# Performance work log

Measured on AMD Instinct MI355X. Metric: run time of the kernel, lower is better.

The kernel has to match this reference:

```python
import jax, jax.numpy as jnp
import numpy as np
import math

NUM_HEADS = 32
NUM_KV_HEADS = 8
HEAD_DIM = 128
SCALE = 1.0 / math.sqrt(128.0)
MAX_SEQLEN = 1152  # static max sequence length for padding
CU = [0, 1024, 1920, 3072, 4096]  # cumulative seq lens, batch=4
NUM_SLOTS = 8192  # 32 blocks * block_size 256


def setup_inputs() -> dict:
    key = jax.random.key(0)
    k0, k1, k2 = jax.random.split(key, 3)
    T = CU[-1]
    q = jax.random.normal(k0, (T, NUM_HEADS, HEAD_DIM), jnp.float32)
    k = jax.random.normal(k1, (T, NUM_KV_HEADS, HEAD_DIM), jnp.float32)
    v = jax.random.normal(k2, (T, NUM_KV_HEADS, HEAD_DIM), jnp.float32)
    k_cache = jnp.zeros((NUM_SLOTS, NUM_KV_HEADS, HEAD_DIM), jnp.float32)
    v_cache = jnp.zeros((NUM_SLOTS, NUM_KV_HEADS, HEAD_DIM), jnp.float32)
    cu_seqlens = jnp.array(CU, dtype=jnp.int32)
    slot_mapping = jnp.arange(T, dtype=jnp.int32)
    return {"q": q, "k": k, "v": v, "k_cache": k_cache, "v_cache": v_cache,
            "cu_seqlens": cu_seqlens, "slot_mapping": slot_mapping}


def _store_kv(key, value, k_cache, v_cache, slot_mapping):
    # scatter new K/V into paged cache; slot == -1 means skip
    valid = slot_mapping >= 0
    safe = jnp.where(valid, slot_mapping, 0)
    k_cache = k_cache.at[safe].set(
        jnp.where(valid[:, None, None], key, k_cache[safe]), mode='drop')
    v_cache = v_cache.at[safe].set(
        jnp.where(valid[:, None, None], value, v_cache[safe]), mode='drop')
    return k_cache, v_cache


def _prefill_attention(q, k, v, cu_seqlens):
    T = q.shape[0]
    B = cu_seqlens.shape[0] - 1
    groups = NUM_HEADS // NUM_KV_HEADS
    k = jnp.repeat(k, groups, axis=1)  # GQA expand -> [T, H, D]
    v = jnp.repeat(v, groups, axis=1)

    lens = cu_seqlens[1:] - cu_seqlens[:-1]            # [B]
    s = jnp.arange(MAX_SEQLEN)
    idx = cu_seqlens[:-1][:, None] + s[None, :]        # [B, S] packed token index
    valid = s[None, :] < lens[:, None]                 # [B, S]
    idx_safe = jnp.where(valid, idx, 0)

    # pack -> padded [B, S, H, D], zeroing pad positions
    qp = jnp.where(valid[..., None, None], q[idx_safe], 0.0)
    kp = jnp.where(valid[..., None, None], k[idx_safe], 0.0)
    vp = jnp.where(valid[..., None, None], v[idx_safe], 0.0)

    scores = jnp.einsum('bqhd,bkhd->bhqk', qp, kp) * SCALE  # [B, H, S, S]
    causal = s[:, None] >= s[None, :]                       # [S, S]
    mask = (causal[None, :, :] & valid[:, :, None] & valid[:, None, :])[:, None, :, :]
    scores = jnp.where(mask, scores, jnp.finfo(scores.dtype).min)
    attn = jax.nn.softmax(scores, axis=-1)
    outp = jnp.einsum('bhqk,bkhd->bqhd', attn, vp)          # [B, S, H, D]

    # unpack padded -> packed [T, H, D]
    tok = jnp.arange(T)
    seq_id = jnp.searchsorted(cu_seqlens, tok, side='right') - 1
    pos = tok - cu_seqlens[seq_id]
    return outp[seq_id, pos]


def reference(q, k, v, k_cache, v_cache, cu_seqlens, slot_mapping):
    k_cache, v_cache = _store_kv(k, v, k_cache, v_cache, slot_mapping)
    out = _prefill_attention(q, k, v, cu_seqlens)
    return out, k_cache, v_cache
```

## Files before the change

kernel.cpp:

```cpp
#include <hip/hip_runtime.h>
#include <hip/hip_bf16.h>

#define T_TOT   4096
#define NH      32
#define NKV     8
#define GQ      4
#define DHEAD   128
#define NSLOTS  8192
#define QB      64
#define QW      32
#define KVB     64
#define NTILES  (T_TOT / KVB)
#define ATT_SCALE 0.088388347648318447f

typedef __attribute__((ext_vector_type(8))) short bf16x8;
typedef __attribute__((ext_vector_type(4))) float f32x4;

__device__ __forceinline__ unsigned short f2bf(float f) {
    union { float f; unsigned u; } x; x.f = f;
    unsigned r = x.u + 0x7fffu + ((x.u >> 16) & 1u);
    return (unsigned short)(r >> 16);
}

__device__ __forceinline__ unsigned long long pack4bf(float a, float b, float c, float d) {
    unsigned lo = (unsigned)f2bf(a) | ((unsigned)f2bf(b) << 16);
    unsigned hi = (unsigned)f2bf(c) | ((unsigned)f2bf(d) << 16);
    return (unsigned long long)lo | ((unsigned long long)hi << 32);
}

__device__ __forceinline__ void gload16(const char* g, char* l) {
    __builtin_amdgcn_global_load_lds(
        (const __attribute__((address_space(1))) void*)g,
        (__attribute__((address_space(3))) void*)l,
        16, 0, 0);
}

__constant__ unsigned char QORD[64] = {
    47,46,15,45,63,14,44,62,13,29,43,61,12,28,42,60,
    11,27,41,59,10,26,40,58, 9,25,39,57, 8,24,38,56,
     7,23,37,55, 6,22,36,54, 5,21,35,53, 4,20,34,52,
     3,19,33,51, 2,18,32,50, 1,17,31,49, 0,16,30,48
};


__global__ __launch_bounds__(256) void copy_cache(const float4* __restrict__ kc,
                                                  const float4* __restrict__ vc,
                                                  float4* __restrict__ kco,
                                                  float4* __restrict__ vco) {
    int idx = blockIdx.x * 256 + threadIdx.x;
    kco[idx] = kc[idx];
    vco[idx] = vc[idx];
}

__global__ __launch_bounds__(256) void scatter_kv(const float4* __restrict__ k,
                                                  const float4* __restrict__ v,
                                                  const int* __restrict__ slot_map,
                                                  float4* __restrict__ kco,
                                                  float4* __restrict__ vco) {
    int idx = blockIdx.x * 256 + threadIdx.x;
    int tok = idx >> 8;
    int j   = idx & 255;
    int slot = slot_map[tok];
    if (slot >= 0 && slot < NSLOTS) {
        size_t dst = (size_t)slot * 256 + j;
        kco[dst] = k[idx];
        vco[dst] = v[idx];
    }
}


__global__ __launch_bounds__(256) void prep_kv(const float* __restrict__ kg,
                                               const float* __restrict__ vg,
                                               char* __restrict__ kbf,
                                               char* __restrict__ vbf) {
    const int tile = blockIdx.x;
    const int kvh  = blockIdx.y;
    const int tid  = threadIdx.x;
    char* kt = kbf + (((size_t)kvh * NTILES + tile) << 14);
    char* vt = vbf + (((size_t)kvh * NTILES + tile) << 14);
    #pragma unroll
    for (int it = 0; it < 8; ++it) {
        int idx = tid + it * 256;
        int key = idx >> 5, d4 = idx & 31;
        float4 x = *(const float4*)(kg +
            ((size_t)(tile * 64 + key) * NKV + kvh) * DHEAD + d4 * 4);
        *(unsigned long long*)(kt + key * 256 + ((d4 * 8) ^ ((key & 7) << 4))) =
            pack4bf(x.x, x.y, x.z, x.w);
    }
    #pragma unroll
    for (int it = 0; it < 8; ++it) {
        int job = tid + it * 256;
        int kq = job >> 7, d = job & 127;
        const float* vp = vg +
            ((size_t)(tile * 64 + kq * 4) * NKV + kvh) * DHEAD + d;
        *(unsigned long long*)(vt + d * 128 + ((kq * 8) ^ ((d & 15) << 3))) =
            pack4bf(vp[0], vp[NKV * DHEAD], vp[2 * NKV * DHEAD], vp[3 * NKV * DHEAD]);
    }
}


__global__ __launch_bounds__(512, 2) void attn_kernel(const float* __restrict__ qg,
                                                      const char* __restrict__ kbf,
                                                      const char* __restrict__ vbf,
                                                      const int* __restrict__ cu,
                                                      float* __restrict__ outg)
{
    __shared__ __align__(16) char Klds[KVB * 256];
    __shared__ __align__(16) char Vt[DHEAD * 128];
    __shared__ __align__(16) char Plds[8][QW * 128];

    const int tid  = threadIdx.x;
    const int wave = tid >> 6;
    const int lane = tid & 63;
    const int q16  = lane & 15;
    const int grp  = lane >> 4;
    const int bid  = blockIdx.x;
    const int qblk = QORD[bid >> 3];
    const int kvh  = bid & 7;
    const int head = kvh * GQ + (wave >> 1);
    const int tok0 = qblk * QB;
    const int qw0  = tok0 + (wave & 1) * QW;

    int seq_start = 0;
    #pragma unroll
    for (int b = 0; b < 4; ++b) {
        int c0 = cu[b], c1 = cu[b + 1];
        if (tok0 >= c0 && tok0 < c1) seq_start = c0;
    }
    const int p0  = tok0 - seq_start;
    const int pw0 = p0 + (wave & 1) * QW;
    const int ntiles = p0 / KVB + 1;
    const int tile0 = seq_start >> 6;

    bf16x8 qf[2][4];
    {
        const float* qp = qg + ((size_t)(qw0 + q16) * NH + head) * DHEAD + grp * 8;
        #pragma unroll
        for (int qt = 0; qt < 2; ++qt) {
            #pragma unroll
            for (int c = 0; c < 4; ++c) {
                const float* p = qp + (size_t)qt * 16 * NH * DHEAD + c * 32;
                float4 a = *(const float4*)(p);
                float4 b = *(const float4*)(p + 4);
                union { bf16x8 v; unsigned long long q[2]; } u;
                u.q[0] = pack4bf(a.x, a.y, a.z, a.w);
                u.q[1] = pack4bf(b.x, b.y, b.z, b.w);
                qf[qt][c] = u.v;
            }
        }
    }

    f32x4 oacc[2][8];
    #pragma unroll
    for (int qt = 0; qt < 2; ++qt)
        #pragma unroll
        for (int n = 0; n < 8; ++n) oacc[qt][n] = (f32x4){0.f, 0.f, 0.f, 0.f};
    float mrow[2][4], lrow[2][4];
    #pragma unroll
    for (int qt = 0; qt < 2; ++qt)
        #pragma unroll
        for (int r = 0; r < 4; ++r) { mrow[qt][r] = -1e30f; lrow[qt][r] = 0.f; }

    char* Pw = Plds[wave];
    const int wbase = wave * 2048;

    for (int t = 0; t < ntiles; ++t) {
        const int k0 = t * KVB;
        const char* gK = kbf + (((size_t)kvh * NTILES + tile0 + t) << 14);
        const char* gV = vbf + (((size_t)kvh * NTILES + tile0 + t) << 14);
        __syncthreads();
        #pragma unroll
        for (int i = 0; i < 2; ++i) {
            gload16(gK + wbase + i * 1024 + lane * 16, Klds + wbase + i * 1024);
            gload16(gV + wbase + i * 1024 + lane * 16, Vt   + wbase + i * 1024);
        }
        __syncthreads();

        float sv[2][4][4];
        const bool lastt = (t == ntiles - 1);
        __builtin_amdgcn_s_setprio(1);
        #pragma unroll
        for (int ktile = 0; ktile < 4; ++ktile) {
            f32x4 sacc0 = (f32x4){0.f, 0.f, 0.f, 0.f};
            f32x4 sacc1 = (f32x4){0.f, 0.f, 0.f, 0.f};
            int row = ktile * 16 + q16;
            #pragma unroll
            for (int c = 0; c < 4; ++c) {
                bf16x8 kf = *(bf16x8*)(Klds + row * 256 +
                                       ((c * 64 + grp * 16) ^ ((row & 7) << 4)));
                sacc0 = __builtin_amdgcn_mfma_f32_16x16x32_bf16(qf[0][c], kf, sacc0, 0, 0, 0);
                sacc1 = __builtin_amdgcn_mfma_f32_16x16x32_bf16(qf[1][c], kf, sacc1, 0, 0, 0);
            }
            if (lastt) {
                int kpos = k0 + ktile * 16 + q16;
                #pragma unroll
                for (int r = 0; r < 4; ++r) {
                    int qp0 = pw0 + grp * 4 + r;
                    sv[0][ktile][r] = (kpos <= qp0)      ? sacc0[r] * ATT_SCALE : -1e30f;
                    sv[1][ktile][r] = (kpos <= qp0 + 16) ? sacc1[r] * ATT_SCALE : -1e30f;
                }
            } else {
                #pragma unroll
                for (int r = 0; r < 4; ++r) {
                    sv[0][ktile][r] = sacc0[r] * ATT_SCALE;
                    sv[1][ktile][r] = sacc1[r] * ATT_SCALE;
                }
            }
        }
        __builtin_amdgcn_s_setprio(0);

        #pragma unroll
        for (int qt = 0; qt < 2; ++qt) {
            #pragma unroll
            for (int r = 0; r < 4; ++r) {
                float tm = fmaxf(fmaxf(sv[qt][0][r], sv[qt][1][r]),
                                 fmaxf(sv[qt][2][r], sv[qt][3][r]));
                #pragma unroll
                for (int mm = 1; mm < 16; mm <<= 1) tm = fmaxf(tm, __shfl_xor(tm, mm));
                if (__any(tm > mrow[qt][r] + 8.0f)) {
                    float newm = fmaxf(tm, mrow[qt][r]);
                    float scal = __expf(mrow[qt][r] - newm);
                    mrow[qt][r] = newm;
                    lrow[qt][r] *= scal;
                    #pragma unroll
                    for (int n = 0; n < 8; ++n) oacc[qt][n][r] *= scal;
                }
                float m = mrow[qt][r];
                float ps = 0.f;
                int qrow = qt * 16 + grp * 4 + r;
                #pragma unroll
                for (int kt2 = 0; kt2 < 4; ++kt2) {
                    float e = __expf(sv[qt][kt2][r] - m);
                    ps += e;
                    *(unsigned short*)(Pw + qrow * 128 +
                        (((kt2 * 16 + q16) * 2) ^ ((qrow & 7) << 4))) = f2bf(e);
                }
                #pragma unroll
                for (int mm = 1; mm < 16; mm <<= 1) ps += __shfl_xor(ps, mm);
                lrow[qt][r] += ps;
            }
        }

        __builtin_amdgcn_s_setprio(1);
        #pragma unroll
        for (int kt = 0; kt < 2; ++kt) {
            bf16x8 pf[2];
            #pragma unroll
            for (int qt = 0; qt < 2; ++qt) {
                int qrow = qt * 16 + q16;
                pf[qt] = *(bf16x8*)(Pw + qrow * 128 +
                                    ((kt * 64 + grp * 16) ^ ((qrow & 7) << 4)));
            }
            #pragma unroll
            for (int n = 0; n < 8; ++n) {
                int d = n * 16 + q16;
                int kq0 = kt * 8 + grp * 2;
                union { bf16x8 v8; unsigned long long q[2]; } uv;
                uv.q[0] = *(unsigned long long*)(Vt + d * 128 + ((kq0 * 8) ^ ((d & 15) << 3)));
                uv.q[1] = *(unsigned long long*)(Vt + d * 128 + (((kq0 + 1) * 8) ^ ((d & 15) << 3)));
                oacc[0][n] = __builtin_amdgcn_mfma_f32_16x16x32_bf16(pf[0], uv.v8, oacc[0][n], 0, 0, 0);
                oacc[1][n] = __builtin_amdgcn_mfma_f32_16x16x32_bf16(pf[1], uv.v8, oacc[1][n], 0, 0, 0);
            }
        }
        __builtin_amdgcn_s_setprio(0);
    }

    #pragma unroll
    for (int qt = 0; qt < 2; ++qt) {
        #pragma unroll
        for (int r = 0; r < 4; ++r) {
            float inv = 1.0f / lrow[qt][r];
            float* op = outg + ((size_t)(qw0 + qt * 16 + grp * 4 + r) * NH + head) * DHEAD;
            #pragma unroll
            for (int n = 0; n < 8; ++n) op[n * 16 + q16] = oacc[qt][n][r] * inv;
        }
    }
}


extern "C" void kernel_launch(void* const* d_in, const int* in_sizes, int n_in,
                              void* d_out, int out_size, void* d_ws, size_t ws_size,
                              hipStream_t stream) {
    const float* q  = (const float*)d_in[0];
    const float* k  = (const float*)d_in[1];
    const float* v  = (const float*)d_in[2];
    const float* kc = (const float*)d_in[3];
    const float* vc = (const float*)d_in[4];
    const int* cu   = (const int*)d_in[5];
    const int* slot = (const int*)d_in[6];

    float* out    = (float*)d_out;
    float* kc_out = out + (size_t)T_TOT * NH * DHEAD;
    float* vc_out = kc_out + (size_t)NSLOTS * NKV * DHEAD;

    char* kbf = (char*)kc_out;
    char* vbf = (char*)vc_out;

    prep_kv<<<dim3(NTILES, NKV), dim3(256), 0, stream>>>(k, v, kbf, vbf);
    attn_kernel<<<dim3(512), dim3(512), 0, stream>>>(q, kbf, vbf, cu, out);

    copy_cache<<<dim3((NSLOTS * NKV * DHEAD / 4) / 256), dim3(256), 0, stream>>>(
        (const float4*)kc, (const float4*)vc, (float4*)kc_out, (float4*)vc_out);
    scatter_kv<<<dim3((T_TOT * NKV * DHEAD / 4) / 256), dim3(256), 0, stream>>>(
        (const float4*)k, (const float4*)v, slot, (float4*)kc_out, (float4*)vc_out);
}
```

Measured before the change: 353.5 us.

## Double-buffer K/V tiles, fold scale into Q, use exp2, defer row-sum reduction

K and V tiles are now double-buffered in LDS, so the next tile's global-to-LDS load is issued before computing on the current one, with a single barrier per iteration. The softmax scale times log2(e) is folded into Q at load time so exp2f replaces __expf and the per-score multiply goes away. The row-sum shuffle reduction moves out of the loop to the epilogue. Other changes: the V-transpose swizzle now matches K's pattern so V fragments load with one 16-byte read, the P buffer shrinks to one 16-row tile per q-subtile, launch bounds rise to 4 blocks per SM, and the q-block schedule order changes. The larger K/V buffers and higher occupancy target increase LDS and register pressure and may cause spills.

```diff
diff --git a/kernel.cpp b/kernel.cpp
--- a/kernel.cpp
+++ b/kernel.cpp
@@ -11,7 +11,7 @@
 #define QW      32
 #define KVB     64
 #define NTILES  (T_TOT / KVB)
-#define ATT_SCALE 0.088388347648318447f
+#define ATT_SCALE_L2E 0.1275174394375425f
 
 typedef __attribute__((ext_vector_type(8))) short bf16x8;
 typedef __attribute__((ext_vector_type(4))) float f32x4;
@@ -38,8 +38,8 @@
 __constant__ unsigned char QORD[64] = {
     47,46,15,45,63,14,44,62,13,29,43,61,12,28,42,60,
     11,27,41,59,10,26,40,58, 9,25,39,57, 8,24,38,56,
-     7,23,37,55, 6,22,36,54, 5,21,35,53, 4,20,34,52,
-     3,19,33,51, 2,18,32,50, 1,17,31,49, 0,16,30,48
+    48,30,16, 0,49,31,17, 1,50,32,18, 2,51,33,19, 3,
+    52,34,20, 4,53,35,21, 5,54,36,22, 6,55,37,23, 7
 };
 
 
@@ -93,21 +93,21 @@
         int kq = job >> 7, d = job & 127;
         const float* vp = vg +
             ((size_t)(tile * 64 + kq * 4) * NKV + kvh) * DHEAD + d;
-        *(unsigned long long*)(vt + d * 128 + ((kq * 8) ^ ((d & 15) << 3))) =
+        *(unsigned long long*)(vt + d * 128 + ((kq * 8) ^ ((d & 7) << 4))) =
             pack4bf(vp[0], vp[NKV * DHEAD], vp[2 * NKV * DHEAD], vp[3 * NKV * DHEAD]);
     }
 }
 
 
-__global__ __launch_bounds__(512, 2) void attn_kernel(const float* __restrict__ qg,
+__global__ __launch_bounds__(512, 4) void attn_kernel(const float* __restrict__ qg,
                                                       const char* __restrict__ kbf,
                                                       const char* __restrict__ vbf,
                                                       const int* __restrict__ cu,
                                                       float* __restrict__ outg)
 {
-    __shared__ __align__(16) char Klds[KVB * 256];
-    __shared__ __align__(16) char Vt[DHEAD * 128];
-    __shared__ __align__(16) char Plds[8][QW * 128];
+    __shared__ __align__(16) char Klds[2][KVB * 256];
+    __shared__ __align__(16) char Vt[2][DHEAD * 128];
+    __shared__ __align__(16) char Plds[8][16 * 128];
 
     const int tid  = threadIdx.x;
     const int wave = tid >> 6;
@@ -131,6 +131,7 @@
     const int pw0 = p0 + (wave & 1) * QW;
     const int ntiles = p0 / KVB + 1;
     const int tile0 = seq_start >> 6;
+    const size_t tbase = (size_t)kvh * NTILES + tile0;
 
     bf16x8 qf[2][4];
     {
@@ -143,8 +144,10 @@
                 float4 a = *(const float4*)(p);
                 float4 b = *(const float4*)(p + 4);
                 union { bf16x8 v; unsigned long long q[2]; } u;
-                u.q[0] = pack4bf(a.x, a.y, a.z, a.w);
-                u.q[1] = pack4bf(b.x, b.y, b.z, b.w);
+                u.q[0] = pack4bf(a.x * ATT_SCALE_L2E, a.y * ATT_SCALE_L2E,
+                                 a.z * ATT_SCALE_L2E, a.w * ATT_SCALE_L2E);
+                u.q[1] = pack4bf(b.x * ATT_SCALE_L2E, b.y * ATT_SCALE_L2E,
+                                 b.z * ATT_SCALE_L2E, b.w * ATT_SCALE_L2E);
                 qf[qt][c] = u.v;
             }
         }
@@ -164,20 +167,36 @@
     char* Pw = Plds[wave];
     const int wbase = wave * 2048;
 
+    {
+        const char* gK = kbf + (tbase << 14);
+        const char* gV = vbf + (tbase << 14);
+        #pragma unroll
+        for (int i = 0; i < 2; ++i) {
+            gload16(gK + wbase + i * 1024 + lane * 16, &Klds[0][0] + wbase + i * 1024);
+            gload16(gV + wbase + i * 1024 + lane * 16, &Vt[0][0]   + wbase + i * 1024);
+        }
+    }
+    __syncthreads();
+
     for (int t = 0; t < ntiles; ++t) {
+        const int buf = t & 1;
+        if (t + 1 < ntiles) {
+            const char* gK = kbf + ((tbase + t + 1) << 14);
+            const char* gV = vbf + ((tbase + t + 1) << 14);
+            char* Kd = &Klds[buf ^ 1][0] + wbase;
+            char* Vd = &Vt[buf ^ 1][0]   + wbase;
+            #pragma unroll
+            for (int i = 0; i < 2; ++i) {
+                gload16(gK + wbase + i * 1024 + lane * 16, Kd + i * 1024);
+                gload16(gV + wbase + i * 1024 + lane * 16, Vd + i * 1024);
+            }
+        }
+        const char* Kb = &Klds[buf][0];
+        const char* Vb = &Vt[buf][0];
         const int k0 = t * KVB;
-        const char* gK = kbf + (((size_t)kvh * NTILES + tile0 + t) << 14);
-        const char* gV = vbf + (((size_t)kvh * NTILES + tile0 + t) << 14);
-        __syncthreads();
-        #pragma unroll
-        for (int i = 0; i < 2; ++i) {
-            gload16(gK + wbase + i * 1024 + lane * 16, Klds + wbase + i * 1024);
-            gload16(gV + wbase + i * 1024 + lane * 16, Vt   + wbase + i * 1024);
-        }
-        __syncthreads();
+        const bool lastt = (t == ntiles - 1);
 
         float sv[2][4][4];
-        const bool lastt = (t == ntiles - 1);
         __builtin_amdgcn_s_setprio(1);
         #pragma unroll
         for (int ktile = 0; ktile < 4; ++ktile) {
@@ -186,7 +205,7 @@
             int row = ktile * 16 + q16;
             #pragma unroll
             for (int c = 0; c < 4; ++c) {
-                bf16x8 kf = *(bf16x8*)(Klds + row * 256 +
+                bf16x8 kf = *(bf16x8*)(Kb + row * 256 +
                                        ((c * 64 + grp * 16) ^ ((row & 7) << 4)));
                 sacc0 = __builtin_amdgcn_mfma_f32_16x16x32_bf16(qf[0][c], kf, sacc0, 0, 0, 0);
                 sacc1 = __builtin_amdgcn_mfma_f32_16x16x32_bf16(qf[1][c], kf, sacc1, 0, 0, 0);
@@ -196,14 +215,14 @@
                 #pragma unroll
                 for (int r = 0; r < 4; ++r) {
                     int qp0 = pw0 + grp * 4 + r;
-                    sv[0][ktile][r] = (kpos <= qp0)      ? sacc0[r] * ATT_SCALE : -1e30f;
-                    sv[1][ktile][r] = (kpos <= qp0 + 16) ? sacc1[r] * ATT_SCALE : -1e30f;
+                    sv[0][ktile][r] = (kpos <= qp0)      ? sacc0[r] : -1e30f;
+                    sv[1][ktile][r] = (kpos <= qp0 + 16) ? sacc1[r] : -1e30f;
                 }
             } else {
                 #pragma unroll
                 for (int r = 0; r < 4; ++r) {
-                    sv[0][ktile][r] = sacc0[r] * ATT_SCALE;
-                    sv[1][ktile][r] = sacc1[r] * ATT_SCALE;
+                    sv[0][ktile][r] = sacc0[r];
+                    sv[1][ktile][r] = sacc1[r];
                 }
             }
         }
@@ -213,13 +232,13 @@
         for (int qt = 0; qt < 2; ++qt) {
             #pragma unroll
             for (int r = 0; r < 4; ++r) {
-                float tm = fmaxf(fmaxf(sv[qt][0][r], sv[qt][1][r]),
-                                 fmaxf(sv[qt][2][r], sv[qt][3][r]));
+                float tm = fmaxf(fmaxf(fmaxf(sv[qt][0][r], sv[qt][1][r]),
+                                 sv[qt][2][r]), sv[qt][3][r]);
                 #pragma unroll
                 for (int mm = 1; mm < 16; mm <<= 1) tm = fmaxf(tm, __shfl_xor(tm, mm));
                 if (__any(tm > mrow[qt][r] + 8.0f)) {
                     float newm = fmaxf(tm, mrow[qt][r]);
-                    float scal = __expf(mrow[qt][r] - newm);
+                    float scal = exp2f(mrow[qt][r] - newm);
                     mrow[qt][r] = newm;
                     lrow[qt][r] *= scal;
                     #pragma unroll
@@ -227,49 +246,44 @@
                 }
                 float m = mrow[qt][r];
                 float ps = 0.f;
-                int qrow = qt * 16 + grp * 4 + r;
+                int qrow = grp * 4 + r;
                 #pragma unroll
                 for (int kt2 = 0; kt2 < 4; ++kt2) {
-                    float e = __expf(sv[qt][kt2][r] - m);
+                    float e = exp2f(sv[qt][kt2][r] - m);
                     ps += e;
                     *(unsigned short*)(Pw + qrow * 128 +
                         (((kt2 * 16 + q16) * 2) ^ ((qrow & 7) << 4))) = f2bf(e);
                 }
-                #pragma unroll
-                for (int mm = 1; mm < 16; mm <<= 1) ps += __shfl_xor(ps, mm);
                 lrow[qt][r] += ps;
             }
-        }
-
-        __builtin_amdgcn_s_setprio(1);
-        #pragma unroll
-        for (int kt = 0; kt < 2; ++kt) {
-            bf16x8 pf[2];
-            #pragma unroll
-            for (int qt = 0; qt < 2; ++qt) {
-                int qrow = qt * 16 + q16;
-                pf[qt] = *(bf16x8*)(Pw + qrow * 128 +
-                                    ((kt * 64 + grp * 16) ^ ((qrow & 7) << 4)));
-            }
-            #pragma unroll
-            for (int n = 0; n < 8; ++n) {
-                int d = n * 16 + q16;
-                int kq0 = kt * 8 + grp * 2;
-                union { bf16x8 v8; unsigned long long q[2]; } uv;
-                uv.q[0] = *(unsigned long long*)(Vt + d * 128 + ((kq0 * 8) ^ ((d & 15) << 3)));
-                uv.q[1] = *(unsigned long long*)(Vt + d * 128 + (((kq0 + 1) * 8) ^ ((d & 15) << 3)));
-                oacc[0][n] = __builtin_amdgcn_mfma_f32_16x16x32_bf16(pf[0], uv.v8, oacc[0][n], 0, 0, 0);
-                oacc[1][n] = __builtin_amdgcn_mfma_f32_16x16x32_bf16(pf[1], uv.v8, oacc[1][n], 0, 0, 0);
-            }
-        }
-        __builtin_amdgcn_s_setprio(0);
+
+            __builtin_amdgcn_s_setprio(1);
+            #pragma unroll
+            for (int kt = 0; kt < 2; ++kt) {
+                bf16x8 pf = *(bf16x8*)(Pw + q16 * 128 +
+                                       ((kt * 64 + grp * 16) ^ ((q16 & 7) << 4)));
+                #pragma unroll
+                for (int n = 0; n < 8; ++n) {
+                    int d = n * 16 + q16;
+                    bf16x8 vv = *(bf16x8*)(Vb + d * 128 +
+                                           ((kt * 64 + grp * 16) ^ ((d & 7) << 4)));
+                    oacc[qt][n] = __builtin_amdgcn_mfma_f32_16x16x32_bf16(pf, vv, oacc[qt][n], 0, 0, 0);
+                }
+            }
+            __builtin_amdgcn_s_setprio(0);
+        }
+
+        __syncthreads();
     }
 
     #pragma unroll
     for (int qt = 0; qt < 2; ++qt) {
         #pragma unroll
         for (int r = 0; r < 4; ++r) {
-            float inv = 1.0f / lrow[qt][r];
+            float ls = lrow[qt][r];
+            #pragma unroll
+            for (int mm = 1; mm < 16; mm <<= 1) ls += __shfl_xor(ls, mm);
+            float inv = 1.0f / ls;
             float* op = outg + ((size_t)(qw0 + qt * 16 + grp * 4 + r) * NH + head) * DHEAD;
             #pragma unroll
             for (int n = 0; n < 8; ++n) op[n * 16 + q16] = oacc[qt][n][r] * inv;
```

Result: slower. 683.5 us (+93.3%).
